# Kernel optimization log

Measured on AMD Instinct MI355X. Metric: run time of the kernel, lower is better.

The kernel has to match this reference:

```python
import jax, jax.numpy as jnp
import numpy as np

VOCAB = 34004
EMB = 300
UNITS = 512


def setup_inputs() -> dict:
    key = jax.random.key(0)
    ks = jax.random.split(key, 16)
    s = 0.05
    B, T_in, T_out = 64, 60, 31
    inp = {
        "dec_input": jax.random.randint(ks[0], (B, T_out), 0, VOCAB, dtype=jnp.int64 if jax.config.jax_enable_x64 else jnp.int32),
        "h0": jax.random.normal(ks[1], (B, UNITS), jnp.float32),
        "c0": jax.random.normal(ks[2], (B, UNITS), jnp.float32),
        "memory": jax.random.normal(ks[3], (B, T_in, UNITS), jnp.float32),
        # embedding table
        "embedding": jax.random.normal(ks[4], (VOCAB, EMB), jnp.float32) * s,
        # LSTM cell: input = concat(emb, prev_attention) -> EMB + UNITS
        "Wk": jax.random.normal(ks[5], (EMB + UNITS, 4 * UNITS), jnp.float32) * s,
        "Uk": jax.random.normal(ks[6], (UNITS, 4 * UNITS), jnp.float32) * s,
        "bk": jnp.zeros((4 * UNITS,), jnp.float32),
        # Bahdanau attention: memory layer, query layer, score vector v
        "Wm": jax.random.normal(ks[7], (UNITS, UNITS), jnp.float32) * s,
        "Wq": jax.random.normal(ks[8], (UNITS, UNITS), jnp.float32) * s,
        "v_att": jax.random.normal(ks[9], (UNITS,), jnp.float32) * s,
        # attention_layer (Dense(dec_units, use_bias=False)) on concat(cell_out, context)
        "Wa": jax.random.normal(ks[10], (2 * UNITS, UNITS), jnp.float32) * s,
        # output projection fc to vocab
        "Wfc": jax.random.normal(ks[11], (UNITS, VOCAB), jnp.float32) * s,
        "bfc": jnp.zeros((VOCAB,), jnp.float32),
    }
    return inp


def reference(dec_input, h0, c0, memory, embedding, Wk, Uk, bk, Wm, Wq, v_att, Wa, Wfc, bfc):
    # Teacher-forced (training=True) AttentionWrapper decode with Bahdanau attention.
    keys = jnp.einsum("btd,de->bte", memory, Wm)  # precompute memory projection [B,T_in,U]
    emb = embedding[dec_input]                      # [B,T_out,EMB]
    emb_t = jnp.swapaxes(emb, 0, 1)                 # [T_out,B,EMB]
    attn0 = jnp.zeros_like(h0)                      # initial attention is zeros

    def step(carry, e):
        h, c, attn = carry
        x = jnp.concatenate([e, attn], axis=-1)     # default cell_input_fn: concat
        z = x @ Wk + h @ Uk + bk                    # [B,4U]
        i, f, g, o = jnp.split(z, 4, axis=-1)       # keras LSTM gate order i,f,c,o
        i = jax.nn.sigmoid(i); f = jax.nn.sigmoid(f)
        g = jnp.tanh(g); o = jax.nn.sigmoid(o)
        c_new = f * c + i * g
        h_new = o * jnp.tanh(c_new)
        # Bahdanau score: v^T tanh(W_m*memory + W_q*query)
        q = h_new @ Wq                               # [B,U]
        score = jnp.einsum("btu,u->bt", jnp.tanh(keys + q[:, None, :]), v_att)
        align = jax.nn.softmax(score, axis=-1)       # [B,T_in]
        context = jnp.einsum("bt,btd->bd", align, memory)
        attn_new = jnp.concatenate([h_new, context], axis=-1) @ Wa  # attention_layer
        logits = attn_new @ Wfc + bfc                # output_layer (fc)
        return (h_new, c_new, attn_new), logits

    _, logits = jax.lax.scan(step, (h0, c0, attn0), emb_t)
    return jnp.swapaxes(logits, 0, 1)               # [B, T_out, vocab] = rnn_output
```

## Files before the change

### kernel.cpp

```cpp
#include <hip/hip_runtime.h>
#include <cstdint>
#include <cstddef>

typedef _Float16 f16;
typedef _Float16 f16x8 __attribute__((ext_vector_type(8)));
typedef _Float16 f16x2 __attribute__((ext_vector_type(2)));
typedef float    f32x4 __attribute__((ext_vector_type(4)));

#define DEV static __device__ __forceinline__

constexpr int TOUT = 31;
constexpr int VOC  = 34004;
constexpr int VOCP = 34048;

constexpr size_t OFF_SYNC  = 0;
constexpr size_t OFF_MEM16 = 8192;
constexpr size_t OFF_WMSWZ = OFF_MEM16 + (size_t)3840*512*2;
constexpr size_t OFF_KEYS  = OFF_WMSWZ + (size_t)16*512*32*2;
constexpr size_t OFF_EMBA  = OFF_KEYS  + (size_t)3840*512*2;
constexpr size_t OFF_WKTOP = OFF_EMBA  + (size_t)1984*320*2;
constexpr size_t OFF_EMBW  = OFF_WKTOP + (size_t)10*2048*32*2;
constexpr size_t OFF_WA16  = OFF_EMBW  + (size_t)1984*2048*4;
constexpr size_t OFF_WKATT = OFF_WA16  + (size_t)1024*512*2;
constexpr size_t OFF_WCA   = OFF_WKATT + (size_t)16*2048*32*2;
constexpr size_t OFF_WSTAR = OFF_WCA   + (size_t)1024*2048*4;
constexpr size_t OFF_UK16  = OFF_WSTAR + (size_t)32*2048*32*2;
constexpr size_t OFF_WQSWZ = OFF_UK16  + (size_t)16*2048*32*2;
constexpr size_t OFF_WASWZ = OFF_WQSWZ + (size_t)512*512*2;
constexpr size_t OFF_H016  = OFF_WASWZ + (size_t)32*512*32*2;
constexpr size_t OFF_YALL  = OFF_H016  + (size_t)64*512*2;
constexpr size_t OFF_ATT16 = OFF_YALL  + (size_t)31*64*1024*2;
constexpr size_t OFF_BKP   = OFF_ATT16 + (size_t)1984*512*2;
constexpr size_t OFF_WFC   = OFF_BKP   + 8192;
constexpr size_t OFF_QP    = OFF_EMBA;

DEV void gload16(const void* src, void* ldsbase ) {
  __builtin_amdgcn_global_load_lds(
      (const __attribute__((address_space(1))) unsigned int*)src,
      (__attribute__((address_space(3))) unsigned int*)ldsbase, 16, 0, 0);
}

DEV float sigm(float x)      { return 1.f / (1.f + expf(-x)); }
DEV float tanh_fast(float x) { float e = __expf(2.f*x); return 1.f - 2.f/(e+1.f); }

DEV uint32_t aload_u32(const uint32_t* p){ return __hip_atomic_load(p, __ATOMIC_RELAXED, __HIP_MEMORY_SCOPE_AGENT); }
DEV float    aload_f32(const float* p)   { return __hip_atomic_load(p, __ATOMIC_RELAXED, __HIP_MEMORY_SCOPE_AGENT); }
DEV void astore_u32(uint32_t* p, uint32_t v){ __hip_atomic_store(p, v, __ATOMIC_RELAXED, __HIP_MEMORY_SCOPE_AGENT); }
DEV void astore_f32(float* p, float v)      { __hip_atomic_store(p, v, __ATOMIC_RELAXED, __HIP_MEMORY_SCOPE_AGENT); }

DEV uint32_t pack16(f16 a, f16 b){ f16x2 v; v[0]=a; v[1]=b; return __builtin_bit_cast(uint32_t, v); }

__global__ void prep_elem(char* ws, const int* dec, const float* h0,
                          const float* memory, const float* embt,
                          const float* Wa, const float* bk)
{
  f16* mem16 = (f16*)(ws+OFF_MEM16);
  f16* embA  = (f16*)(ws+OFF_EMBA);
  f16* wa16  = (f16*)(ws+OFF_WA16);
  f16* h016  = (f16*)(ws+OFF_H016);
  float* bkp = (float*)(ws+OFF_BKP);
  constexpr int E0=1966080, E1=E0+634880, E2=E1+524288, E3=E2+32768, E4=E3+2048;
  for (int i = blockIdx.x*256 + threadIdx.x; i < E4; i += gridDim.x*256) {
    if (i < E0) { mem16[i] = (f16)memory[i]; }
    else if (i < E1) { int j=i-E0; int r=j/320, k=j-r*320; int t=r>>6, b=r&63;
      int tok = dec[b*TOUT+t];
      embA[j] = (k<300) ? (f16)embt[(size_t)tok*300+k] : (f16)0.f; }
    else if (i < E2) { int j=i-E1; wa16[j] = (f16)Wa[j]; }
    else if (i < E3) { int j=i-E2; h016[j] = (f16)h0[j]; }
    else { int j=i-E3; bkp[j] = bk[(j>>2) + (j&3)*512]; }
  }
}

__global__ void prep_swz(char* ws, const float* Wm, const float* Wk, const float* Uk,
                         const float* Wa, const float* Wq)
{
  int tg = blockIdx.x*256 + threadIdx.x;
  constexpr int S0=8192, S1=S0+20480, S2=S1+32768, S3=S2+32768, S4=S3+16384, S5=S4+8192;
  if (tg >= S5) return;
  f16 buf[32];
  f16* dst;
  if (tg < S0) {
    int kt=tg>>9, n=tg&511;
    #pragma unroll
    for (int kk=0;kk<32;kk++) buf[kk] = (f16)Wm[(size_t)(kt*32+kk)*512 + n];
    dst = (f16*)(ws+OFF_WMSWZ) + (size_t)tg*32;
  } else if (tg < S1) {
    int j=tg-S0; int kt=j>>11, np=j&2047; int col=(np>>2)+(np&3)*512;
    #pragma unroll
    for (int kk=0;kk<32;kk++){ int k=kt*32+kk;
      buf[kk] = (k<300) ? (f16)Wk[(size_t)k*2048+col] : (f16)0.f; }
    dst = (f16*)(ws+OFF_WKTOP) + (size_t)j*32;
  } else if (tg < S2) {
    int j=tg-S1; int kt=j>>11, np=j&2047; int col=(np>>2)+(np&3)*512;
    #pragma unroll
    for (int kk=0;kk<32;kk++) buf[kk] = (f16)Wk[(size_t)(300+kt*32+kk)*2048+col];
    dst = (f16*)(ws+OFF_WKATT) + (size_t)j*32;
  } else if (tg < S3) {
    int j=tg-S2; int kt=j>>11, np=j&2047; int col=(np>>2)+(np&3)*512;
    #pragma unroll
    for (int kk=0;kk<32;kk++) buf[kk] = (f16)Uk[(size_t)(kt*32+kk)*2048+col];
    dst = (f16*)(ws+OFF_UK16) + (size_t)j*32;
  } else if (tg < S4) {
    int j=tg-S3; int kt=j>>9, n=j&511;
    #pragma unroll
    for (int kk=0;kk<32;kk++) buf[kk] = (f16)Wa[(size_t)(kt*32+kk)*512 + n];
    dst = (f16*)(ws+OFF_WASWZ) + (size_t)j*32;
  } else {
    int j=tg-S4; int rr=j>>9, n=j&511;
    #pragma unroll
    for (int kk=0;kk<32;kk++) buf[kk] = (f16)Wq[(size_t)(rr*32+kk)*512 + n];
    dst = (f16*)(ws+OFF_WQSWZ) + (size_t)j*32;
  }
  f16x8* d8 = (f16x8*)dst; f16x8* s8 = (f16x8*)buf;
  d8[0]=s8[0]; d8[1]=s8[1]; d8[2]=s8[2]; d8[3]=s8[3];
}

__global__ void prep_wfc(char* ws, const float* Wfc)
{
  int n  = blockIdx.x*256 + threadIdx.x;
  int kt = blockIdx.y;
  f16 buf[32];
  #pragma unroll
  for (int kk=0;kk<32;kk++)
    buf[kk] = (n < VOC) ? (f16)Wfc[(size_t)(kt*32+kk)*VOC + n] : (f16)0.f;
  f16* dst = (f16*)(ws+OFF_WFC) + ((size_t)kt*VOCP + n)*32;
  f16x8* d8 = (f16x8*)dst; f16x8* s8 = (f16x8*)buf;
  d8[0]=s8[0]; d8[1]=s8[1]; d8[2]=s8[2]; d8[3]=s8[3];
}

__global__ void build_wstar(char* ws, const float* Uk)
{
  int tg = blockIdx.x*256 + threadIdx.x;
  int kt = tg>>11, np = tg&2047;
  int col = (np>>2)+(np&3)*512;
  const float* wca = (const float*)(ws+OFF_WCA);
  f16 buf[32];
  #pragma unroll
  for (int kk=0;kk<32;kk++){
    int k = kt*32+kk;
    float v = wca[(size_t)k*2048 + np];
    if (k < 512) v += Uk[(size_t)k*2048 + col];
    buf[kk] = (f16)v;
  }
  f16* dst = (f16*)(ws+OFF_WSTAR) + (size_t)tg*32;
  f16x8* d8 = (f16x8*)dst; f16x8* s8 = (f16x8*)buf;
  d8[0]=s8[0]; d8[1]=s8[1]; d8[2]=s8[2]; d8[3]=s8[3];
}

template<int BM, int BN, int WR, int WC, int MODE>
__global__ __launch_bounds__(WR*WC*64, 1)
void gemm16(const f16* __restrict__ A, int lda,
            const f16* __restrict__ Bs, int Np,
            void* __restrict__ C, const float* __restrict__ bias,
            int M, int K, int Mreal, int Nreal)
{
  constexpr int NT  = WR*WC*64;
  constexpr int WTM = BM/WR, WTN = BN/WC, AM = WTM/16, AN = WTN/16;
  constexpr int NLA = BM*64/(NT*16), NLB = BN*64/(NT*16);
  __shared__ __align__(16) f16 sA[BM*32];
  __shared__ __align__(16) f16 sB[BN*32];
  const int tid = threadIdx.x, wave = tid>>6, lane = tid&63;
  const int lg = lane>>4, lr = lane&15;
  const int m0 = blockIdx.y*BM, n0 = blockIdx.x*BN;
  const int wm = (wave/WC)*WTM, wn = (wave%WC)*WTN;

  f32x4 acc[AM][AN] = {};

  int aoff[AM], boff[AN];
  #pragma unroll
  for (int i=0;i<AM;i++){ int row = wm+i*16+lr; aoff[i] = row*64 + (((lg + (row>>1))&3)<<4); }
  #pragma unroll
  for (int i=0;i<AN;i++){ int row = wn+i*16+lr; boff[i] = row*64 + (((lg + (row>>1))&3)<<4); }

  const int ksteps = K/32;
  for (int ks=0; ks<ksteps; ks++){
    const int k0 = ks*32;
    __syncthreads();
    #pragma unroll
    for (int i=0;i<NLA;i++){
      int p = i*NT + tid;
      int row = p>>2; int g = ((p&3) - (row>>1)) & 3;
      int gm = m0+row; if (gm > Mreal-1) gm = Mreal-1;
      gload16(A + (size_t)gm*lda + k0 + g*8, (char*)sA + (i*NT + wave*64)*16);
    }
    #pragma unroll
    for (int i=0;i<NLB;i++){
      int p = i*NT + tid;
      int row = p>>2; int g = ((p&3) - (row>>1)) & 3;
      gload16(Bs + ((size_t)(k0>>5)*Np + (n0+row))*32 + g*8, (char*)sB + (i*NT + wave*64)*16);
    }
    __syncthreads();
    f16x8 af[AM], bf[AN];
    #pragma unroll
    for (int i=0;i<AM;i++) af[i] = *(const f16x8*)((const char*)sA + aoff[i]);
    #pragma unroll
    for (int i=0;i<AN;i++) bf[i] = *(const f16x8*)((const char*)sB + boff[i]);
    #pragma unroll
    for (int i=0;i<AM;i++)
      #pragma unroll
      for (int j=0;j<AN;j++)
        acc[i][j] = __builtin_amdgcn_mfma_f32_16x16x32_f16(af[i], bf[j], acc[i][j], 0,0,0);
  }

  #pragma unroll
  for (int i=0;i<AM;i++)
    #pragma unroll
    for (int j=0;j<AN;j++){
      int n = n0 + wn + j*16 + lr;
      if (MODE == 2 && n >= Nreal) continue;
      float bb = 0.f;
      if (MODE != 1 && bias) bb = bias[n];
      #pragma unroll
      for (int r=0;r<4;r++){
        int m = m0 + wm + i*16 + lg*4 + r;
        if (m >= Mreal) continue;
        float v = acc[i][j][r] + bb;
        if (MODE == 0)      ((float*)C)[(size_t)m*Np + n] = v;
        else if (MODE == 1) ((f16*)C)[(size_t)m*Np + n] = (f16)v;
        else { int t = m>>6, b = m&63; ((float*)C)[((size_t)(b*TOUT+t))*VOC + n] = v; }
      }
    }
}

DEV void cbar(uint32_t* flags, int cbase, int r, int tid, uint32_t target)
{
  asm volatile("s_waitcnt vmcnt(0)" ::: "memory");
  __syncthreads();
  if (tid == 0)
    astore_u32(flags + (size_t)(cbase + r)*32, target);
  if (tid < 16) {
    while (aload_u32(flags + (size_t)(cbase + tid)*32) < target)
      __builtin_amdgcn_s_sleep(1);
  }
  __syncthreads();
}

template<int KS>
DEV f32x4 p1_mfma(const f16* __restrict__ Bs, const char* ylb, int col, int kg, int lr)
{
  f16x8 B[8];
  #pragma unroll
  for (int i=0;i<8;i++)
    B[i] = *(const f16x8*)(Bs + (((size_t)i*2048 + col)<<5) + kg*8);
  f32x4 acc = {};
  #pragma unroll
  for (int ks=0; ks<KS; ks+=8) {
    #pragma unroll
    for (int i=0;i<8;i++) {
      f16x8 a = *(const f16x8*)(ylb + lr*2064 + (ks+i)*64 + kg*16);
      acc = __builtin_amdgcn_mfma_f32_16x16x32_f16(a, B[i], acc, 0,0,0);
      int nk = ks+8+i;
      if (nk < KS)
        B[i] = *(const f16x8*)(Bs + (((size_t)nk*2048 + col)<<5) + kg*8);
    }
  }
  return acc;
}

__global__ __launch_bounds__(512, 1)
void recur(char* ws, const float* __restrict__ c0, const float* __restrict__ v_att)
{
  const int blk = blockIdx.x, tid = threadIdx.x;
  const int wave = tid>>6, lane = tid&63;
  const int lr = lane&15, kg = lane>>4;
  const int clus = blk>>4, r = blk&15;
  const int cbase = clus<<4;
  const int bown = cbase + r;
  const int n0 = r*128;

  uint32_t* flags = (uint32_t*)(ws+OFF_SYNC);
  float* qp = (float*)(ws+OFF_QP);
  const f16* wstar = (const f16*)(ws+OFF_WSTAR);
  const f16* uk16  = (const f16*)(ws+OFF_UK16);
  const f16* wqswz = (const f16*)(ws+OFF_WQSWZ);
  const f16* keys16= (const f16*)(ws+OFF_KEYS);
  const f16* mem16 = (const f16*)(ws+OFF_MEM16);
  const float* embw= (const float*)(ws+OFF_EMBW);

  __shared__ __align__(16) char  yl[16*2064];
  __shared__ __align__(16) float zl[16*132];
  __shared__ __align__(16) float c_sl[16*32];
  __shared__ __align__(16) f16   h_sl[16*32];
  __shared__ __align__(16) float q_l[512];
  __shared__ __align__(16) float v_l[512];
  __shared__ __align__(16) f16   cx16_l[512];
  __shared__ __align__(16) float sc_l[64];

  v_l[tid] = v_att[tid];
  { int b = tid>>5, uu = tid&31;
    c_sl[b*32+uu] = c0[(size_t)(cbase+b)*512 + r*32 + uu]; }

  for (int t=0; t<TOUT; t++){
    {
      const uint32_t* ysrc; int rw;
      if (t == 0) { ysrc = (const uint32_t*)(ws+OFF_H016); rw = 256; }
      else        { ysrc = (const uint32_t*)(ws+OFF_YALL + (size_t)(t-1)*64*1024*2); rw = 512; }
      if (tid < rw) {
        uint32_t g[16];
        #pragma unroll
        for (int q=0;q<16;q++) g[q] = aload_u32(ysrc + (size_t)(cbase+q)*rw + tid);
        #pragma unroll
        for (int q=0;q<16;q++) *(uint32_t*)(yl + q*2064 + tid*4) = g[q];
      }
      __syncthreads();
    }

    {
      const int col = n0 + wave*16 + lr;
      f32x4 acc = (t==0) ? p1_mfma<16>(uk16,  yl, col, kg, lr)
                         : p1_mfma<32>(wstar, yl, col, kg, lr);
      #pragma unroll
      for (int rr=0;rr<4;rr++)
        zl[(kg*4+rr)*132 + wave*16 + lr] = acc[rr];
    }
    __syncthreads();

    {
      const int b = tid>>5, uu = tid&31;
      f32x4 zz = *(const f32x4*)(zl + b*132 + uu*4);
      f32x4 e  = *(const f32x4*)(embw + ((size_t)(t*64+cbase+b))*2048 + n0 + uu*4);
      float ig = sigm(zz[0]+e[0]), fg = sigm(zz[1]+e[1]);
      float gg = tanhf(zz[2]+e[2]), og = sigm(zz[3]+e[3]);
      float cn = fg*c_sl[b*32+uu] + ig*gg;
      c_sl[b*32+uu] = cn;
      h_sl[b*32+uu] = (f16)(og * tanhf(cn));
    }
    __syncthreads();

    uint32_t* yt = (uint32_t*)(ws+OFF_YALL) + (size_t)t*64*512;
    if (tid < 256) {
      int b = tid>>4, j = tid&15;
      astore_u32(yt + (size_t)(cbase+b)*512 + r*16 + j,
                 pack16(h_sl[b*32+2*j], h_sl[b*32+2*j+1]));
    }
    {
      f16x8 a = *(const f16x8*)(h_sl + lr*32 + kg*8);
      #pragma unroll
      for (int j=0;j<4;j++){
        int n = wave*64 + j*16 + lr;
        f16x8 bf = *(const f16x8*)(wqswz + ((size_t)(r*512 + n))*32 + kg*8);
        f32x4 aq = __builtin_amdgcn_mfma_f32_16x16x32_f16(a, bf, (f32x4){0.f,0.f,0.f,0.f}, 0,0,0);
        #pragma unroll
        for (int rr=0;rr<4;rr++)
          astore_f32(qp + ((size_t)blk*16 + kg*4+rr)*512 + n, aq[rr]);
      }
    }
    cbar(flags, cbase, r, tid, 2*t+1);

    {
      float pv[16];
      #pragma unroll
      for (int s=0;s<16;s++)
        pv[s] = aload_f32(qp + ((size_t)(cbase+s)*16 + r)*512 + tid);
      float qs = 0.f;
      #pragma unroll
      for (int s=0;s<16;s++) qs += pv[s];
      q_l[tid] = qs;
    }
    __syncthreads();

    for (int i = wave; i < 60; i += 8){
      const f16* krow = keys16 + ((size_t)(bown*60+i))*512;
      float p = 0.f;
      #pragma unroll
      for (int s=0;s<8;s++){
        int u = lane + s*64;
        p += tanh_fast((float)krow[u] + q_l[u]) * v_l[u];
      }
      #pragma unroll
      for (int m=32;m;m>>=1) p += __shfl_xor(p, m, 64);
      if (lane == 0) sc_l[i] = p;
    }
    __syncthreads();
    if (wave == 0){
      float s = (lane < 60) ? sc_l[lane] : -1e30f;
      float mx = s;
      #pragma unroll
      for (int m=32;m;m>>=1) mx = fmaxf(mx, __shfl_xor(mx, m, 64));
      float ev = (lane < 60) ? __expf(s - mx) : 0.f;
      float sum = ev;
      #pragma unroll
      for (int m=32;m;m>>=1) sum += __shfl_xor(sum, m, 64);
      if (lane < 60) sc_l[lane] = ev / sum;
    }
    __syncthreads();
    {
      float cx = 0.f;
      const f16* mrow = mem16 + ((size_t)bown*60)*512 + tid;
      #pragma unroll 4
      for (int i=0;i<60;i++) cx += sc_l[i] * (float)mrow[(size_t)i*512];
      cx16_l[tid] = (f16)cx;
    }
    __syncthreads();
    if (tid < 256)
      astore_u32(yt + (size_t)bown*512 + 256 + tid,
                 pack16(cx16_l[2*tid], cx16_l[2*tid+1]));
    cbar(flags, cbase, r, tid, 2*t+2);
  }
}

extern "C" void kernel_launch(void* const* d_in, const int* in_sizes, int n_in,
                              void* d_out, int out_size, void* d_ws, size_t ws_size,
                              hipStream_t stream)
{
  const int*   dec  = (const int*)  d_in[0];
  const float* h0   = (const float*)d_in[1];
  const float* c0   = (const float*)d_in[2];
  const float* mem  = (const float*)d_in[3];
  const float* embt = (const float*)d_in[4];
  const float* Wk   = (const float*)d_in[5];
  const float* Uk   = (const float*)d_in[6];
  const float* bk   = (const float*)d_in[7];
  const float* Wm   = (const float*)d_in[8];
  const float* Wq   = (const float*)d_in[9];
  const float* va   = (const float*)d_in[10];
  const float* Wa   = (const float*)d_in[11];
  const float* Wfc  = (const float*)d_in[12];
  const float* bfc  = (const float*)d_in[13];
  char* ws = (char*)d_ws;

  hipMemsetAsync(ws + OFF_SYNC, 0, 8192, stream);

  prep_elem<<<4096, 256, 0, stream>>>(ws, dec, h0, mem, embt, Wa, bk);
  prep_swz <<<464, 256, 0, stream>>>(ws, Wm, Wk, Uk, Wa, Wq);
  prep_wfc <<<dim3(133,16), 256, 0, stream>>>(ws, Wfc);

  gemm16<128,64,2,2,1><<<dim3(8,30), 256, 0, stream>>>(
      (const f16*)(ws+OFF_MEM16), 512, (const f16*)(ws+OFF_WMSWZ), 512,
      ws+OFF_KEYS, nullptr, 3840, 512, 3840, 512);
  gemm16<128,64,2,2,0><<<dim3(32,16), 256, 0, stream>>>(
      (const f16*)(ws+OFF_EMBA), 320, (const f16*)(ws+OFF_WKTOP), 2048,
      ws+OFF_EMBW, (const float*)(ws+OFF_BKP), 1984, 320, 1984, 2048);
  gemm16<128,64,2,2,0><<<dim3(32,8), 256, 0, stream>>>(
      (const f16*)(ws+OFF_WA16), 512, (const f16*)(ws+OFF_WKATT), 2048,
      ws+OFF_WCA, nullptr, 1024, 512, 1024, 2048);
  build_wstar<<<256, 256, 0, stream>>>(ws, Uk);

  recur<<<64, 512, 0, stream>>>(ws, c0, va);

  gemm16<128,64,2,2,1><<<dim3(8,16), 256, 0, stream>>>(
      (const f16*)(ws+OFF_YALL), 1024, (const f16*)(ws+OFF_WASWZ), 512,
      ws+OFF_ATT16, nullptr, 1984, 1024, 1984, 512);
  gemm16<128,256,2,4,2><<<dim3(133,16), 512, 0, stream>>>(
      (const f16*)(ws+OFF_ATT16), 512, (const f16*)(ws+OFF_WFC), VOCP,
      d_out, bfc, 1984, 512, 1984, VOC);
}
```

Before: 890.2 us.

## Vectorize recurrent-kernel global exchanges, cache memory rows in LDS, retile vocab GEMM

The recurrent kernel now moves its per-step cross-block data (previous hidden/context rows, partial query sums) with 16-byte global loads and stores carrying the sc1 cache bit, replacing scalar relaxed atomic accesses. Query partials are staged in LDS and written out as coalesced vectors. Each block also preloads its 60x512 fp16 memory slice into LDS once, so the per-step context reduction reads LDS instead of global memory. Separately, the final vocab projection GEMM swaps its tile shape from 128x256 to 256x128. The risks are coherence correctness with the sc1 inline asm and the larger LDS footprint.

Result: faster. 836.6 us (-6.0%).

```diff
diff --git a/kernel.cpp b/kernel.cpp
--- a/kernel.cpp
+++ b/kernel.cpp
@@ -6,6 +6,7 @@
 typedef _Float16 f16x8 __attribute__((ext_vector_type(8)));
 typedef _Float16 f16x2 __attribute__((ext_vector_type(2)));
 typedef float    f32x4 __attribute__((ext_vector_type(4)));
+typedef uint32_t u32x4 __attribute__((ext_vector_type(4)));
 
 #define DEV static __device__ __forceinline__
 
@@ -44,11 +45,15 @@
 DEV float tanh_fast(float x) { float e = __expf(2.f*x); return 1.f - 2.f/(e+1.f); }
 
 DEV uint32_t aload_u32(const uint32_t* p){ return __hip_atomic_load(p, __ATOMIC_RELAXED, __HIP_MEMORY_SCOPE_AGENT); }
-DEV float    aload_f32(const float* p)   { return __hip_atomic_load(p, __ATOMIC_RELAXED, __HIP_MEMORY_SCOPE_AGENT); }
 DEV void astore_u32(uint32_t* p, uint32_t v){ __hip_atomic_store(p, v, __ATOMIC_RELAXED, __HIP_MEMORY_SCOPE_AGENT); }
-DEV void astore_f32(float* p, float v)      { __hip_atomic_store(p, v, __ATOMIC_RELAXED, __HIP_MEMORY_SCOPE_AGENT); }
-
-DEV uint32_t pack16(f16 a, f16 b){ f16x2 v; v[0]=a; v[1]=b; return __builtin_bit_cast(uint32_t, v); }
+
+DEV void ld16_sc1(const void* p, u32x4& d){
+  asm volatile("global_load_dwordx4 %0, %1, off sc1" : "=v"(d) : "v"(p));
+}
+DEV void st16_sc1(void* p, u32x4 v){
+  asm volatile("global_store_dwordx4 %0, %1, off sc1" :: "v"(p), "v"(v) : "memory");
+}
+DEV void vwait(){ asm volatile("s_waitcnt vmcnt(0)" ::: "memory"); }
 
 __global__ void prep_elem(char* ws, const int* dec, const float* h0,
                           const float* memory, const float* embt,
@@ -224,7 +229,7 @@
 
 DEV void cbar(uint32_t* flags, int cbase, int r, int tid, uint32_t target)
 {
-  asm volatile("s_waitcnt vmcnt(0)" ::: "memory");
+  vwait();
   __syncthreads();
   if (tid == 0)
     astore_u32(flags + (size_t)(cbase + r)*32, target);
@@ -269,7 +274,7 @@
   const int n0 = r*128;
 
   uint32_t* flags = (uint32_t*)(ws+OFF_SYNC);
-  float* qp = (float*)(ws+OFF_QP);
+  char* qpg = (char*)(ws+OFF_QP);
   const f16* wstar = (const f16*)(ws+OFF_WSTAR);
   const f16* uk16  = (const f16*)(ws+OFF_UK16);
   const f16* wqswz = (const f16*)(ws+OFF_WQSWZ);
@@ -277,38 +282,59 @@
   const f16* mem16 = (const f16*)(ws+OFF_MEM16);
   const float* embw= (const float*)(ws+OFF_EMBW);
 
-  __shared__ __align__(16) char  yl[16*2064];
+  __shared__ __align__(16) char  ybuf[33024];
   __shared__ __align__(16) float zl[16*132];
-  __shared__ __align__(16) float c_sl[16*32];
-  __shared__ __align__(16) f16   h_sl[16*32];
+  __shared__ __align__(16) float c_sl[512];
+  __shared__ __align__(16) f16   h_sl[512];
   __shared__ __align__(16) float q_l[512];
   __shared__ __align__(16) float v_l[512];
   __shared__ __align__(16) f16   cx16_l[512];
   __shared__ __align__(16) float sc_l[64];
+  __shared__ __align__(16) f16   mem_lds[60*512];
 
   v_l[tid] = v_att[tid];
   { int b = tid>>5, uu = tid&31;
-    c_sl[b*32+uu] = c0[(size_t)(cbase+b)*512 + r*32 + uu]; }
+    c_sl[tid] = c0[(size_t)(cbase+b)*512 + r*32 + uu]; }
+
+  {
+    const char* msrc = (const char*)(mem16 + (size_t)bown*60*512);
+    #pragma unroll
+    for (int i=0;i<8;i++){
+      int cb = i*512 + wave*64;
+      if (cb < 3840)
+        gload16(msrc + ((size_t)cb + lane)*16, (char*)mem_lds + (size_t)cb*16);
+    }
+  }
 
   for (int t=0; t<TOUT; t++){
     {
-      const uint32_t* ysrc; int rw;
-      if (t == 0) { ysrc = (const uint32_t*)(ws+OFF_H016); rw = 256; }
-      else        { ysrc = (const uint32_t*)(ws+OFF_YALL + (size_t)(t-1)*64*1024*2); rw = 512; }
-      if (tid < rw) {
-        uint32_t g[16];
-        #pragma unroll
-        for (int q=0;q<16;q++) g[q] = aload_u32(ysrc + (size_t)(cbase+q)*rw + tid);
-        #pragma unroll
-        for (int q=0;q<16;q++) *(uint32_t*)(yl + q*2064 + tid*4) = g[q];
+      const char* ysrc; int rsh;
+      if (t == 0) { ysrc = ws+OFF_H016; rsh = 6; }
+      else        { ysrc = ws+OFF_YALL + (size_t)(t-1)*64*2048; rsh = 7; }
+      const int npass = (16 << rsh) >> 9;
+      u32x4 g[4];
+      #pragma unroll
+      for (int p=0;p<4;p++){
+        if (p < npass){
+          int cid = p*512 + tid, row = cid>>rsh, off = cid & ((1<<rsh)-1);
+          ld16_sc1(ysrc + ((size_t)(cbase+row) << (rsh+4)) + off*16, g[p]);
+        }
+      }
+      vwait();
+      #pragma unroll
+      for (int p=0;p<4;p++){
+        if (p < npass){
+          int cid = p*512 + tid, row = cid>>rsh, off = cid & ((1<<rsh)-1);
+          *(u32x4*)(ybuf + row*2064 + off*16) = g[p];
+        }
       }
       __syncthreads();
     }
 
     {
       const int col = n0 + wave*16 + lr;
-      f32x4 acc = (t==0) ? p1_mfma<16>(uk16,  yl, col, kg, lr)
-                         : p1_mfma<32>(wstar, yl, col, kg, lr);
+      f32x4 acc = (t==0) ? p1_mfma<16>(uk16,  ybuf, col, kg, lr)
+                         : p1_mfma<32>(wstar, ybuf, col, kg, lr);
       #pragma unroll
       for (int rr=0;rr<4;rr++)
         zl[(kg*4+rr)*132 + wave*16 + lr] = acc[rr];
@@ -321,19 +347,21 @@
       f32x4 e  = *(const f32x4*)(embw + ((size_t)(t*64+cbase+b))*2048 + n0 + uu*4);
       float ig = sigm(zz[0]+e[0]), fg = sigm(zz[1]+e[1]);
       float gg = tanhf(zz[2]+e[2]), og = sigm(zz[3]+e[3]);
-      float cn = fg*c_sl[b*32+uu] + ig*gg;
-      c_sl[b*32+uu] = cn;
-      h_sl[b*32+uu] = (f16)(og * tanhf(cn));
-    }
-    __syncthreads();
-
-    uint32_t* yt = (uint32_t*)(ws+OFF_YALL) + (size_t)t*64*512;
-    if (tid < 256) {
-      int b = tid>>4, j = tid&15;
-      astore_u32(yt + (size_t)(cbase+b)*512 + r*16 + j,
-                 pack16(h_sl[b*32+2*j], h_sl[b*32+2*j+1]));
-    }
-    {
+      float cn = fg*c_sl[tid] + ig*gg;
+      c_sl[tid] = cn;
+      h_sl[tid] = (f16)(og * tanhf(cn));
+    }
+    __syncthreads();
+
+    char* yt = (char*)(ws+OFF_YALL) + (size_t)t*64*2048;
+    if (tid < 64){
+      int b = tid>>2, off = tid&3;
+      u32x4 v = *(const u32x4*)((const char*)h_sl + b*64 + off*16);
+      st16_sc1(yt + (size_t)(cbase+b)*2048 + r*64 + off*16, v);
+    }
+
+    {
+      float* qs = (float*)ybuf;
       f16x8 a = *(const f16x8*)(h_sl + lr*32 + kg*8);
       #pragma unroll
       for (int j=0;j<4;j++){
@@ -342,20 +370,39 @@
         f32x4 aq = __builtin_amdgcn_mfma_f32_16x16x32_f16(a, bf, (f32x4){0.f,0.f,0.f,0.f}, 0,0,0);
         #pragma unroll
         for (int rr=0;rr<4;rr++)
-          astore_f32(qp + ((size_t)blk*16 + kg*4+rr)*512 + n, aq[rr]);
+          qs[(kg*4+rr)*512 + n] = aq[rr];
+      }
+    }
+    __syncthreads();
+    {
+      #pragma unroll
+      for (int p=0;p<4;p++){
+        int cid = p*512 + tid;
+        u32x4 v = *(const u32x4*)(ybuf + cid*16);
+        st16_sc1(qpg + (size_t)blk*32768 + cid*16, v);
       }
     }
     cbar(flags, cbase, r, tid, 2*t+1);
 
     {
-      float pv[16];
-      #pragma unroll
-      for (int s=0;s<16;s++)
-        pv[s] = aload_f32(qp + ((size_t)(cbase+s)*16 + r)*512 + tid);
-      float qs = 0.f;
-      #pragma unroll
-      for (int s=0;s<16;s++) qs += pv[s];
-      q_l[tid] = qs;
+      u32x4 gq[4];
+      #pragma unroll
+      for (int p=0;p<4;p++){
+        int cid = p*512 + tid, s = cid>>7, off = cid&127;
+        ld16_sc1(qpg + (size_t)(cbase+s)*32768 + r*2048 + off*16, gq[p]);
+      }
+      vwait();
+      #pragma unroll
+      for (int p=0;p<4;p++){
+        int cid = p*512 + tid;
+        *(u32x4*)(ybuf + cid*16) = gq[p];
+      }
+      __syncthreads();
+      const float* qin = (const float*)ybuf;
+      float qsum = 0.f;
+      #pragma unroll
+      for (int s=0;s<16;s++) qsum += qin[s*512 + tid];
+      q_l[tid] = qsum;
     }
     __syncthreads();
 
@@ -386,15 +433,15 @@
     __syncthreads();
     {
       float cx = 0.f;
-      const f16* mrow = mem16 + ((size_t)bown*60)*512 + tid;
-      #pragma unroll 4
-      for (int i=0;i<60;i++) cx += sc_l[i] * (float)mrow[(size_t)i*512];
+      #pragma unroll
+      for (int i=0;i<60;i++) cx += sc_l[i] * (float)mem_lds[i*512 + tid];
       cx16_l[tid] = (f16)cx;
     }
     __syncthreads();
-    if (tid < 256)
-      astore_u32(yt + (size_t)bown*512 + 256 + tid,
-                 pack16(cx16_l[2*tid], cx16_l[2*tid+1]));
+    if (tid < 64){
+      u32x4 v = *(const u32x4*)((const char*)cx16_l + tid*16);
+      st16_sc1(yt + (size_t)bown*2048 + 1024 + tid*16, v);
+    }
     cbar(flags, cbase, r, tid, 2*t+2);
   }
 }
@@ -441,7 +488,7 @@
   gemm16<128,64,2,2,1><<<dim3(8,16), 256, 0, stream>>>(
       (const f16*)(ws+OFF_YALL), 1024, (const f16*)(ws+OFF_WASWZ), 512,
       ws+OFF_ATT16, nullptr, 1984, 1024, 1984, 512);
-  gemm16<128,256,2,4,2><<<dim3(133,16), 512, 0, stream>>>(
+  gemm16<256,128,4,2,2><<<dim3(266,8), 512, 0, stream>>>(
       (const f16*)(ws+OFF_ATT16), 512, (const f16*)(ws+OFF_WFC), VOCP,
       d_out, bfc, 1984, 512, 1984, VOC);
 }
```
